# Kernel optimization log

Hardware: AMD Instinct MI355X
Metric: run time of the kernel (lower is better)

The kernel has to match this reference:

```python
import jax, jax.numpy as jnp
import numpy as np

N_NODES = 50000
N_EDGES = 800000


def _gat_conv(x, src, dst, n, W, a_src, a_dst, b, concat):
    # x: [N, Fin]; W: [Fin, H*C]; a_src/a_dst: [H, C]; b: [H*C] or [C]
    H, C = a_src.shape
    h = (x @ W).reshape(n, H, C)                     # [N,H,C]
    alpha_src = jnp.sum(h * a_src[None], axis=-1)    # [N,H]
    alpha_dst = jnp.sum(h * a_dst[None], axis=-1)    # [N,H]
    e = alpha_src[src] + alpha_dst[dst]              # [E,H]
    e = jax.nn.leaky_relu(e, negative_slope=0.2)
    # segment softmax over incoming edges of each dst node
    m = jax.ops.segment_max(e, dst, num_segments=n)  # [N,H]
    ex = jnp.exp(e - m[dst])
    s = jax.ops.segment_sum(ex, dst, num_segments=n)
    alpha = ex / (s[dst] + 1e-16)                    # [E,H]
    msg = h[src] * alpha[:, :, None]                 # [E,H,C]
    out = jax.ops.segment_sum(msg, dst, num_segments=n)  # [N,H,C]
    out = out.reshape(n, H * C) if concat else out.mean(axis=1)
    return out + b


def setup_inputs() -> dict:
    key = jax.random.key(0)
    ks = jax.random.split(key, 12)
    d = {}
    d['x'] = jax.random.normal(ks[0], (N_NODES, 128), dtype=jnp.float32)
    d['edge_index'] = jax.random.randint(ks[1], (2, N_EDGES), 0, N_NODES, dtype=jnp.int32)
    s = 0.1
    d['w1'] = jax.random.normal(ks[2], (128, 128), dtype=jnp.float32) * s
    d['att_src1'] = jax.random.normal(ks[3], (2, 64), dtype=jnp.float32) * s
    d['att_dst1'] = jax.random.normal(ks[4], (2, 64), dtype=jnp.float32) * s
    d['b1'] = jnp.zeros((128,), jnp.float32)
    d['w2'] = jax.random.normal(ks[5], (128, 128), dtype=jnp.float32) * s
    d['att_src2'] = jax.random.normal(ks[6], (2, 64), dtype=jnp.float32) * s
    d['att_dst2'] = jax.random.normal(ks[7], (2, 64), dtype=jnp.float32) * s
    d['b2'] = jnp.zeros((128,), jnp.float32)
    d['w3'] = jax.random.normal(ks[8], (128, 40), dtype=jnp.float32) * s
    d['att_src3'] = jax.random.normal(ks[9], (1, 40), dtype=jnp.float32) * s
    d['att_dst3'] = jax.random.normal(ks[10], (1, 40), dtype=jnp.float32) * s
    d['b3'] = jnp.zeros((40,), jnp.float32)
    return d


def reference(x, edge_index, w1, att_src1, att_dst1, b1,
              w2, att_src2, att_dst2, b2, w3, att_src3, att_dst3, b3):
    n = x.shape[0]
    # PyG GATConv adds self-loops by default
    loop = jnp.arange(n, dtype=edge_index.dtype)
    src = jnp.concatenate([edge_index[0], loop])
    dst = jnp.concatenate([edge_index[1], loop])
    h = _gat_conv(x, src, dst, n, w1, att_src1, att_dst1, b1, concat=True)
    h = jax.nn.elu(h)  # dropout skipped (eval mode)
    h = _gat_conv(h, src, dst, n, w2, att_src2, att_dst2, b2, concat=True)
    h = jax.nn.elu(h)
    out = _gat_conv(h, src, dst, n, w3, att_src3, att_dst3, b3, concat=False)
    return out
```

## Files before the change

### kernel.cpp

```cpp
#include <hip/hip_runtime.h>
#include <hip/hip_fp16.h>

#define NN 50000
#define NE 800000
#define E2 850000
#define SCAN_NB 49
#define GEMM_BLKS 782

static inline int cdiv(long long a, int b) { return (int)((a + b - 1) / b); }

using half8  = __attribute__((ext_vector_type(8))) _Float16;
using floatx4 = __attribute__((ext_vector_type(4))) float;

struct __align__(16) h2x4 { __half2 a, b, c, d; };
struct __align__(8)  h2x2 { __half2 a, b; };

__device__ __forceinline__ void edge_sd(const int* __restrict__ ei, int e, int& s, int& d) {
    if (e < NE) { s = ei[e]; d = ei[NE + e]; }
    else { s = e - NE; d = s; }
}

__global__ __launch_bounds__(256) void prep(const float* __restrict__ x, __half* __restrict__ x16,
                                            const float* __restrict__ w1, __half* __restrict__ wt1,
                                            const float* __restrict__ w2, __half* __restrict__ wt2,
                                            const float* __restrict__ w3, __half* __restrict__ wt3,
                                            int* __restrict__ deg) {
    int tid = blockIdx.x * 256 + threadIdx.x;
    int stride = gridDim.x * 256;
    for (int i = tid; i < NN * 32; i += stride) {
        float4 v = *(const float4*)&x[(size_t)i * 4];
        h2x2 st;
        st.a = __floats2half2_rn(v.x, v.y);
        st.b = __floats2half2_rn(v.z, v.w);
        *(h2x2*)&x16[(size_t)i * 4] = st;
    }
    for (int i = tid; i < 128 * 128; i += stride)
        wt1[i] = __float2half(w1[(i & 127) * 128 + (i >> 7)]);
    for (int i = tid; i < 128 * 128; i += stride)
        wt2[i] = __float2half(w2[(i & 127) * 128 + (i >> 7)]);
    for (int i = tid; i < 40 * 128; i += stride)
        wt3[i] = __float2half(w3[(i & 127) * 40 + (i >> 7)]);
    for (int i = tid; i < NN; i += stride) deg[i] = 0;
}

__global__ __launch_bounds__(256) void rank_pass(const int* __restrict__ ei,
                                                 int* __restrict__ deg,
                                                 int* __restrict__ rank) {
    int e = blockIdx.x * 256 + threadIdx.x;
    if (e >= E2) return;
    int d = (e < NE) ? ei[NE + e] : (e - NE);
    rank[e] = atomicAdd(&deg[d], 1);
}

__global__ __launch_bounds__(256) void scan1(const int* __restrict__ deg,
                                             int* __restrict__ loc,
                                             int* __restrict__ bsums) {
    __shared__ int wsum[4];
    int base = blockIdx.x * 1024 + threadIdx.x * 4;
    int4 v = make_int4(0, 0, 0, 0);
    if (base + 3 < NN) v = *(const int4*)&deg[base];
    else {
        if (base + 0 < NN) v.x = deg[base + 0];
        if (base + 1 < NN) v.y = deg[base + 1];
        if (base + 2 < NN) v.z = deg[base + 2];
    }
    v.y += v.x; v.z += v.y; v.w += v.z;
    int lane = threadIdx.x & 63;
    int wid = threadIdx.x >> 6;
    int t = v.w;
#pragma unroll
    for (int off = 1; off < 64; off <<= 1) {
        int u = __shfl_up(t, off, 64);
        if (lane >= off) t += u;
    }
    int excl = t - v.w;
    if (lane == 63) wsum[wid] = t;
    __syncthreads();
    int woff = 0;
    for (int w = 0; w < wid; ++w) woff += wsum[w];
    int add = excl + woff;
    int4 o = make_int4(v.x + add, v.y + add, v.z + add, v.w + add);
    if (base + 3 < NN) *(int4*)&loc[base] = o;
    else {
        if (base + 0 < NN) loc[base + 0] = o.x;
        if (base + 1 < NN) loc[base + 1] = o.y;
        if (base + 2 < NN) loc[base + 2] = o.z;
    }
    if (threadIdx.x == 255) bsums[blockIdx.x] = add + v.w;
}

__global__ __launch_bounds__(256) void scan23(const int* __restrict__ loc,
                                              const int* __restrict__ bsums,
                                              int* __restrict__ rowp) {
    __shared__ int sh_b[64];
    int tid = threadIdx.x;
    if (tid < 64) {
        int orig = (tid < SCAN_NB) ? bsums[tid] : 0;
        int v = orig;
#pragma unroll
        for (int off = 1; off < 64; off <<= 1) {
            int u = __shfl_up(v, off, 64);
            if (tid >= off) v += u;
        }
        sh_b[tid] = v - orig;
    }
    __syncthreads();
    int i = blockIdx.x * 256 + tid;
    if (i == 0) rowp[0] = 0;
    if (i < NN) rowp[i + 1] = loc[i] + sh_b[i >> 10];
}

template<int MOUT, int H>
__device__ __forceinline__ void gemm_body(int bid, const __half* __restrict__ X,
                                          const __half* __restrict__ WT,
                                          const float* __restrict__ aS,
                                          const float* __restrict__ aD,
                                          __half* __restrict__ Ho,
                                          float* __restrict__ osrc,
                                          float* __restrict__ odst,
                                          __half* wlds) {
    constexpr int NT = (MOUT + 15) / 16;
    constexpr int NR = NT * 16;
    const int tid = threadIdx.x;
    for (int i = tid * 8; i < MOUT * 128; i += 2048) {
        half8 v = *(const half8*)&WT[i];
        *(half8*)&wlds[(i >> 7) * 136 + (i & 127)] = v;
    }
    if (NR > MOUT) {
        for (int i = tid * 8; i < (NR - MOUT) * 128; i += 2048) {
            half8 z = {};
            *(half8*)&wlds[(MOUT + (i >> 7)) * 136 + (i & 127)] = z;
        }
    }
    __syncthreads();

    const int lane = tid & 63;
    const int wid = tid >> 6;
    const int r0 = bid * 64 + wid * 16;
    const int arow = r0 + (lane & 15);
    const int lrow = (arow < NN) ? arow : (NN - 1);
    const int koff = (lane >> 4) * 8;
    const size_t xbase = (size_t)lrow * 128 + koff;
    half8 a0 = *(const half8*)&X[xbase];
    half8 a1 = *(const half8*)&X[xbase + 32];
    half8 a2 = *(const half8*)&X[xbase + 64];
    half8 a3 = *(const half8*)&X[xbase + 96];

    floatx4 acc[NT];
#pragma unroll
    for (int t = 0; t < NT; ++t) acc[t] = (floatx4){0.f, 0.f, 0.f, 0.f};

#pragma unroll
    for (int t = 0; t < NT; ++t) {
        const __half* wp = &wlds[(t * 16 + (lane & 15)) * 136 + koff];
        half8 b0 = *(const half8*)&wp[0];
        half8 b1 = *(const half8*)&wp[32];
        half8 b2 = *(const half8*)&wp[64];
        half8 b3 = *(const half8*)&wp[96];
        acc[t] = __builtin_amdgcn_mfma_f32_16x16x32_f16(a0, b0, acc[t], 0, 0, 0);
        acc[t] = __builtin_amdgcn_mfma_f32_16x16x32_f16(a1, b1, acc[t], 0, 0, 0);
        acc[t] = __builtin_amdgcn_mfma_f32_16x16x32_f16(a2, b2, acc[t], 0, 0, 0);
        acc[t] = __builtin_amdgcn_mfma_f32_16x16x32_f16(a3, b3, acc[t], 0, 0, 0);
    }

    const int cc = lane & 15;
    const int rbase = r0 + (lane >> 4) * 4;
    float ps[H][4], pd[H][4];
#pragma unroll
    for (int h = 0; h < H; ++h)
#pragma unroll
        for (int r = 0; r < 4; ++r) { ps[h][r] = 0.f; pd[h][r] = 0.f; }

#pragma unroll
    for (int t = 0; t < NT; ++t) {
        const int col = t * 16 + cc;
        const bool cv = (col < MOUT);
        const float as_ = cv ? aS[col] : 0.f;
        const float ad_ = cv ? aD[col] : 0.f;
        const int h = (H == 2) ? (t >> 2) : 0;
#pragma unroll
        for (int r = 0; r < 4; ++r) {
            ps[h][r] = fmaf(acc[t][r], as_, ps[h][r]);
            pd[h][r] = fmaf(acc[t][r], ad_, pd[h][r]);
        }
    }

    if constexpr (MOUT == 128) {
        __syncthreads();
        const int rowbase = wid * 16;
#pragma unroll
        for (int t = 0; t < NT; ++t)
#pragma unroll
            for (int r = 0; r < 4; ++r)
                wlds[(rowbase + (lane >> 4) * 4 + r) * 136 + t * 16 + cc] =
                    __float2half(acc[t][r]);
        __syncthreads();
#pragma unroll
        for (int p2 = 0; p2 < 4; ++p2) {
            int f = (p2 * 64 + lane) * 8;
            int row = f >> 7, col = f & 127;
            h2x4 v = *(h2x4*)&wlds[(rowbase + row) * 136 + col];
            int grow = r0 + row;
            if (grow < NN) *(h2x4*)&Ho[(size_t)grow * 128 + col] = v;
        }
    } else {
#pragma unroll
        for (int t = 0; t < NT; ++t) {
            const int col = t * 16 + cc;
            const bool cv = (col < MOUT);
#pragma unroll
            for (int r = 0; r < 4; ++r) {
                const int m = rbase + r;
                if (cv && m < NN) Ho[(size_t)m * MOUT + col] = __float2half(acc[t][r]);
            }
        }
    }

#pragma unroll
    for (int off = 1; off <= 8; off <<= 1) {
#pragma unroll
        for (int h = 0; h < H; ++h)
#pragma unroll
            for (int r = 0; r < 4; ++r) {
                ps[h][r] += __shfl_xor(ps[h][r], off, 64);
                pd[h][r] += __shfl_xor(pd[h][r], off, 64);
            }
    }
    if (cc == 0) {
#pragma unroll
        for (int r = 0; r < 4; ++r) {
            const int m = rbase + r;
            if (m < NN) {
#pragma unroll
                for (int h = 0; h < H; ++h) {
                    osrc[m * H + h] = ps[h][r];
                    odst[m * H + h] = pd[h][r];
                }
            }
        }
    }
}

__global__ __launch_bounds__(256) void gemm16_k128(const __half* __restrict__ X,
                                                   const __half* __restrict__ WT,
                                                   const float* __restrict__ aS,
                                                   const float* __restrict__ aD,
                                                   __half* __restrict__ Ho,
                                                   float* __restrict__ osrc,
                                                   float* __restrict__ odst) {
    __shared__ __half wlds[128 * 136];
    gemm_body<128, 2>(blockIdx.x, X, WT, aS, aD, Ho, osrc, odst, wlds);
}

__global__ __launch_bounds__(256) void gemm16_k40(const __half* __restrict__ X,
                                                  const __half* __restrict__ WT,
                                                  const float* __restrict__ aS,
                                                  const float* __restrict__ aD,
                                                  __half* __restrict__ Ho,
                                                  float* __restrict__ osrc,
                                                  float* __restrict__ odst) {
    __shared__ __half wlds[48 * 136];
    gemm_body<40, 1>(blockIdx.x, X, WT, aS, aD, Ho, osrc, odst, wlds);
}

__global__ __launch_bounds__(256) void gemm1_scat(const __half* __restrict__ X,
                                                  const __half* __restrict__ WT,
                                                  const float* __restrict__ aS,
                                                  const float* __restrict__ aD,
                                                  __half* __restrict__ Ho,
                                                  float* __restrict__ osrc,
                                                  float* __restrict__ odst,
                                                  const int* __restrict__ ei,
                                                  const int* __restrict__ rowp,
                                                  const int* __restrict__ rank,
                                                  int* __restrict__ csr_src) {
    __shared__ __half wlds[128 * 136];
    if (blockIdx.x < GEMM_BLKS) {
        gemm_body<128, 2>(blockIdx.x, X, WT, aS, aD, Ho, osrc, odst, wlds);
        return;
    }
    int e = (blockIdx.x - GEMM_BLKS) * 256 + threadIdx.x;
    if (e >= E2) return;
    int s, d; edge_sd(ei, e, s, d);
    csr_src[rowp[d] + rank[e]] = s;
}

__global__ __launch_bounds__(256) void agg_h2(const int* __restrict__ rowp,
                                              const int* __restrict__ csr_src,
                                              const __half* __restrict__ Hf,
                                              const float* __restrict__ osrc,
                                              const float* __restrict__ odst,
                                              const float* __restrict__ bias,
                                              __half* __restrict__ outp) {
    int n = blockIdx.x * 4 + (threadIdx.x >> 6);
    if (n >= NN) return;
    int lane = threadIdx.x & 63;
    int i0 = rowp[n], i1 = rowp[n + 1];
    int c = lane & 15;
    int slot = lane >> 4;
    int c8 = c * 8;
    int h2 = c >> 3;
    float adh = odst[n * 2 + h2];
    bool pl = ((c & 7) == 0);

    float4 lo0{0.f,0.f,0.f,0.f}, hi0{0.f,0.f,0.f,0.f};
    float4 lo1{0.f,0.f,0.f,0.f}, hi1{0.f,0.f,0.f,0.f};
    float psum = 0.f;

    int idx = i0 + slot;
    for (; idx + 12 < i1; idx += 16) {
        int s0 = csr_src[idx];
        int s1 = csr_src[idx + 4];
        int s2 = csr_src[idx + 8];
        int s3 = csr_src[idx + 12];
        float e0 = osrc[s0 * 2 + h2] + adh;
        float e1 = osrc[s1 * 2 + h2] + adh;
        float e2 = osrc[s2 * 2 + h2] + adh;
        float e3 = osrc[s3 * 2 + h2] + adh;
        e0 = (e0 >= 0.f) ? e0 : 0.2f * e0;
        e1 = (e1 >= 0.f) ? e1 : 0.2f * e1;
        e2 = (e2 >= 0.f) ? e2 : 0.2f * e2;
        e3 = (e3 >= 0.f) ? e3 : 0.2f * e3;
        float p0 = __expf(e0), p1 = __expf(e1), p2 = __expf(e2), p3 = __expf(e3);
        h2x4 hv0 = *(const h2x4*)&Hf[(size_t)s0 * 128 + c8];
        h2x4 hv1 = *(const h2x4*)&Hf[(size_t)s1 * 128 + c8];
        h2x4 hv2 = *(const h2x4*)&Hf[(size_t)s2 * 128 + c8];
        h2x4 hv3 = *(const h2x4*)&Hf[(size_t)s3 * 128 + c8];
        if (pl) psum += (p0 + p1) + (p2 + p3);
        float2 f;
        f = __half22float2(hv0.a); lo0.x = fmaf(f.x, p0, lo0.x); lo0.y = fmaf(f.y, p0, lo0.y);
        f = __half22float2(hv0.b); lo0.z = fmaf(f.x, p0, lo0.z); lo0.w = fmaf(f.y, p0, lo0.w);
        f = __half22float2(hv0.c); hi0.x = fmaf(f.x, p0, hi0.x); hi0.y = fmaf(f.y, p0, hi0.y);
        f = __half22float2(hv0.d); hi0.z = fmaf(f.x, p0, hi0.z); hi0.w = fmaf(f.y, p0, hi0.w);
        f = __half22float2(hv1.a); lo0.x = fmaf(f.x, p1, lo0.x); lo0.y = fmaf(f.y, p1, lo0.y);
        f = __half22float2(hv1.b); lo0.z = fmaf(f.x, p1, lo0.z); lo0.w = fmaf(f.y, p1, lo0.w);
        f = __half22float2(hv1.c); hi0.x = fmaf(f.x, p1, hi0.x); hi0.y = fmaf(f.y, p1, hi0.y);
        f = __half22float2(hv1.d); hi0.z = fmaf(f.x, p1, hi0.z); hi0.w = fmaf(f.y, p1, hi0.w);
        f = __half22float2(hv2.a); lo1.x = fmaf(f.x, p2, lo1.x); lo1.y = fmaf(f.y, p2, lo1.y);
        f = __half22float2(hv2.b); lo1.z = fmaf(f.x, p2, lo1.z); lo1.w = fmaf(f.y, p2, lo1.w);
        f = __half22float2(hv2.c); hi1.x = fmaf(f.x, p2, hi1.x); hi1.y = fmaf(f.y, p2, hi1.y);
        f = __half22float2(hv2.d); hi1.z = fmaf(f.x, p2, hi1.z); hi1.w = fmaf(f.y, p2, hi1.w);
        f = __half22float2(hv3.a); lo1.x = fmaf(f.x, p3, lo1.x); lo1.y = fmaf(f.y, p3, lo1.y);
        f = __half22float2(hv3.b); lo1.z = fmaf(f.x, p3, lo1.z); lo1.w = fmaf(f.y, p3, lo1.w);
        f = __half22float2(hv3.c); hi1.x = fmaf(f.x, p3, hi1.x); hi1.y = fmaf(f.y, p3, hi1.y);
        f = __half22float2(hv3.d); hi1.z = fmaf(f.x, p3, hi1.z); hi1.w = fmaf(f.y, p3, hi1.w);
    }
    for (; idx < i1; idx += 4) {
        int s0 = csr_src[idx];
        float e0 = osrc[s0 * 2 + h2] + adh;
        e0 = (e0 >= 0.f) ? e0 : 0.2f * e0;
        float p0 = __expf(e0);
        h2x4 hv0 = *(const h2x4*)&Hf[(size_t)s0 * 128 + c8];
        if (pl) psum += p0;
        float2 f;
        f = __half22float2(hv0.a); lo0.x = fmaf(f.x, p0, lo0.x); lo0.y = fmaf(f.y, p0, lo0.y);
        f = __half22float2(hv0.b); lo0.z = fmaf(f.x, p0, lo0.z); lo0.w = fmaf(f.y, p0, lo0.w);
        f = __half22float2(hv0.c); hi0.x = fmaf(f.x, p0, hi0.x); hi0.y = fmaf(f.y, p0, hi0.y);
        f = __half22float2(hv0.d); hi0.z = fmaf(f.x, p0, hi0.z); hi0.w = fmaf(f.y, p0, hi0.w);
    }
    float4 lo{lo0.x + lo1.x, lo0.y + lo1.y, lo0.z + lo1.z, lo0.w + lo1.w};
    float4 hi{hi0.x + hi1.x, hi0.y + hi1.y, hi0.z + hi1.z, hi0.w + hi1.w};
#pragma unroll
    for (int off = 16; off <= 32; off <<= 1) {
        lo.x += __shfl_xor(lo.x, off, 64); lo.y += __shfl_xor(lo.y, off, 64);
        lo.z += __shfl_xor(lo.z, off, 64); lo.w += __shfl_xor(lo.w, off, 64);
        hi.x += __shfl_xor(hi.x, off, 64); hi.y += __shfl_xor(hi.y, off, 64);
        hi.z += __shfl_xor(hi.z, off, 64); hi.w += __shfl_xor(hi.w, off, 64);
        psum += __shfl_xor(psum, off, 64);
    }
    float sh = __shfl(psum, h2 * 8, 64);
    float inv = 1.f / (sh + 1e-16f);
    if (lane < 16) {
        float4 bl = *(const float4*)&bias[c8];
        float4 bh = *(const float4*)&bias[c8 + 4];
        float o0 = fmaf(lo.x, inv, bl.x), o1 = fmaf(lo.y, inv, bl.y);
        float o2 = fmaf(lo.z, inv, bl.z), o3 = fmaf(lo.w, inv, bl.w);
        float o4 = fmaf(hi.x, inv, bh.x), o5 = fmaf(hi.y, inv, bh.y);
        float o6 = fmaf(hi.z, inv, bh.z), o7 = fmaf(hi.w, inv, bh.w);
        o0 = (o0 > 0.f) ? o0 : (__expf(o0) - 1.f);
        o1 = (o1 > 0.f) ? o1 : (__expf(o1) - 1.f);
        o2 = (o2 > 0.f) ? o2 : (__expf(o2) - 1.f);
        o3 = (o3 > 0.f) ? o3 : (__expf(o3) - 1.f);
        o4 = (o4 > 0.f) ? o4 : (__expf(o4) - 1.f);
        o5 = (o5 > 0.f) ? o5 : (__expf(o5) - 1.f);
        o6 = (o6 > 0.f) ? o6 : (__expf(o6) - 1.f);
        o7 = (o7 > 0.f) ? o7 : (__expf(o7) - 1.f);
        h2x4 st;
        st.a = __floats2half2_rn(o0, o1);
        st.b = __floats2half2_rn(o2, o3);
        st.c = __floats2half2_rn(o4, o5);
        st.d = __floats2half2_rn(o6, o7);
        *(h2x4*)&outp[(size_t)n * 128 + c8] = st;
    }
}

__global__ __launch_bounds__(256) void agg_h1(const int* __restrict__ rowp,
                                              const int* __restrict__ csr_src,
                                              const __half* __restrict__ Hf,
                                              const float* __restrict__ osrc,
                                              const float* __restrict__ odst,
                                              const float* __restrict__ bias,
                                              float* __restrict__ outp) {
    int n = blockIdx.x * 4 + (threadIdx.x >> 6);
    if (n >= NN) return;
    int lane = threadIdx.x & 63;
    int i0 = rowp[n], i1 = rowp[n + 1];
    float ad = odst[n];
    int c = lane & 15;
    int slot = lane >> 4;
    bool cl = (c < 10);
    bool pl = (c == 0);
    float4 acc0{0.f,0.f,0.f,0.f}, acc1{0.f,0.f,0.f,0.f};
    float psum = 0.f;

    int idx = i0 + slot;
    for (; idx + 12 < i1; idx += 16) {
        int s0 = csr_src[idx];
        int s1 = csr_src[idx + 4];
        int s2 = csr_src[idx + 8];
        int s3 = csr_src[idx + 12];
        float e0 = osrc[s0] + ad, e1 = osrc[s1] + ad;
        float e2 = osrc[s2] + ad, e3 = osrc[s3] + ad;
        e0 = (e0 >= 0.f) ? e0 : 0.2f * e0;
        e1 = (e1 >= 0.f) ? e1 : 0.2f * e1;
        e2 = (e2 >= 0.f) ? e2 : 0.2f * e2;
        e3 = (e3 >= 0.f) ? e3 : 0.2f * e3;
        float p0 = __expf(e0), p1 = __expf(e1), p2 = __expf(e2), p3 = __expf(e3);
        if (pl) psum += (p0 + p1) + (p2 + p3);
        if (cl) {
            h2x2 hv0 = *(const h2x2*)&Hf[(size_t)s0 * 40 + c * 4];
            h2x2 hv1 = *(const h2x2*)&Hf[(size_t)s1 * 40 + c * 4];
            h2x2 hv2 = *(const h2x2*)&Hf[(size_t)s2 * 40 + c * 4];
            h2x2 hv3 = *(const h2x2*)&Hf[(size_t)s3 * 40 + c * 4];
            float2 f;
            f = __half22float2(hv0.a); acc0.x = fmaf(f.x, p0, acc0.x); acc0.y = fmaf(f.y, p0, acc0.y);
            f = __half22float2(hv0.b); acc0.z = fmaf(f.x, p0, acc0.z); acc0.w = fmaf(f.y, p0, acc0.w);
            f = __half22float2(hv1.a); acc1.x = fmaf(f.x, p1, acc1.x); acc1.y = fmaf(f.y, p1, acc1.y);
            f = __half22float2(hv1.b); acc1.z = fmaf(f.x, p1, acc1.z); acc1.w = fmaf(f.y, p1, acc1.w);
            f = __half22float2(hv2.a); acc0.x = fmaf(f.x, p2, acc0.x); acc0.y = fmaf(f.y, p2, acc0.y);
            f = __half22float2(hv2.b); acc0.z = fmaf(f.x, p2, acc0.z); acc0.w = fmaf(f.y, p2, acc0.w);
            f = __half22float2(hv3.a); acc1.x = fmaf(f.x, p3, acc1.x); acc1.y = fmaf(f.y, p3, acc1.y);
            f = __half22float2(hv3.b); acc1.z = fmaf(f.x, p3, acc1.z); acc1.w = fmaf(f.y, p3, acc1.w);
        }
    }
    for (; idx < i1; idx += 4) {
        int s0 = csr_src[idx];
        float e0 = osrc[s0] + ad;
        e0 = (e0 >= 0.f) ? e0 : 0.2f * e0;
        float p0 = __expf(e0);
        if (pl) psum += p0;
        if (cl) {
            h2x2 hv0 = *(const h2x2*)&Hf[(size_t)s0 * 40 + c * 4];
            float2 f;
            f = __half22float2(hv0.a); acc0.x = fmaf(f.x, p0, acc0.x); acc0.y = fmaf(f.y, p0, acc0.y);
            f = __half22float2(hv0.b); acc0.z = fmaf(f.x, p0, acc0.z); acc0.w = fmaf(f.y, p0, acc0.w);
        }
    }
    float4 acc{acc0.x + acc1.x, acc0.y + acc1.y, acc0.z + acc1.z, acc0.w + acc1.w};
#pragma unroll
    for (int off = 16; off <= 32; off <<= 1) {
        acc.x += __shfl_xor(acc.x, off, 64);
        acc.y += __shfl_xor(acc.y, off, 64);
        acc.z += __shfl_xor(acc.z, off, 64);
        acc.w += __shfl_xor(acc.w, off, 64);
        psum += __shfl_xor(psum, off, 64);
    }
    float sh = __shfl(psum, 0, 64);
    float inv = 1.f / (sh + 1e-16f);
    if (lane < 10) {
        float4 b = *(const float4*)&bias[lane * 4];
        float4 o;
        o.x = fmaf(acc.x, inv, b.x);
        o.y = fmaf(acc.y, inv, b.y);
        o.z = fmaf(acc.z, inv, b.z);
        o.w = fmaf(acc.w, inv, b.w);
        *(float4*)&outp[(size_t)n * 40 + lane * 4] = o;
    }
}

extern "C" void kernel_launch(void* const* d_in, const int* in_sizes, int n_in,
                              void* d_out, int out_size, void* d_ws, size_t ws_size,
                              hipStream_t stream) {
    const float* x   = (const float*)d_in[0];
    const int*   ei  = (const int*)d_in[1];
    const float* w1  = (const float*)d_in[2];
    const float* as1 = (const float*)d_in[3];
    const float* ad1 = (const float*)d_in[4];
    const float* b1  = (const float*)d_in[5];
    const float* w2  = (const float*)d_in[6];
    const float* as2 = (const float*)d_in[7];
    const float* ad2 = (const float*)d_in[8];
    const float* b2  = (const float*)d_in[9];
    const float* w3  = (const float*)d_in[10];
    const float* as3 = (const float*)d_in[11];
    const float* ad3 = (const float*)d_in[12];
    const float* b3  = (const float*)d_in[13];
    float* out = (float*)d_out;

    char* p = (char*)d_ws;
    __half* x16   = (__half*)p; p += (size_t)NN * 128 * 2;
    __half* h16   = (__half*)p; p += (size_t)NN * 128 * 2;
    __half* f16   = (__half*)p; p += (size_t)NN * 128 * 2;
    __half* wt1   = (__half*)p; p += (size_t)128 * 128 * 2;
    __half* wt2   = (__half*)p; p += (size_t)128 * 128 * 2;
    __half* wt3   = (__half*)p; p += (size_t)64 * 128 * 2;
    float*  osrc  = (float*)p;  p += (size_t)NN * 2 * 4;
    float*  odst  = (float*)p;  p += (size_t)NN * 2 * 4;
    int*    rowp  = (int*)p;    p += (size_t)(NN + 1) * 4;
    int*    deg   = (int*)p;    p += (size_t)NN * 4;
    int*    rank  = (int*)p;    p += (size_t)E2 * 4;
    int*    loc   = (int*)p;    p += (size_t)NN * 4;
    int*    bsums = (int*)p;    p += (size_t)64 * 4;
    int*    csrsrc= (int*)p;    p += (size_t)E2 * 4;

    const int edgeGrid = cdiv(E2, 256);
    const int nodeGrid = cdiv(NN, 4);

    prep<<<2048, 256, 0, stream>>>(x, x16, w1, wt1, w2, wt2, w3, wt3, deg);
    rank_pass<<<edgeGrid, 256, 0, stream>>>(ei, deg, rank);
    scan1<<<SCAN_NB, 256, 0, stream>>>(deg, loc, bsums);
    scan23<<<cdiv(NN, 256), 256, 0, stream>>>(loc, bsums, rowp);

    gemm1_scat<<<GEMM_BLKS + edgeGrid, 256, 0, stream>>>(x16, wt1, as1, ad1, h16,
                                                         osrc, odst, ei, rowp, rank, csrsrc);
    agg_h2<<<nodeGrid, 256, 0, stream>>>(rowp, csrsrc, h16, osrc, odst, b1, f16);

    gemm16_k128<<<GEMM_BLKS, 256, 0, stream>>>(f16, wt2, as2, ad2, h16, osrc, odst);
    agg_h2<<<nodeGrid, 256, 0, stream>>>(rowp, csrsrc, h16, osrc, odst, b2, f16);

    gemm16_k40<<<GEMM_BLKS, 256, 0, stream>>>(f16, wt3, as3, ad3, h16, osrc, odst);
    agg_h1<<<nodeGrid, 256, 0, stream>>>(rowp, csrsrc, h16, osrc, odst, b3, out);
}
```

Baseline: 198.8 us.

## Merge prep with rank pass, fuse scan into one kernel, unroll aggregation tails

```diff
diff --git a/kernel.cpp b/kernel.cpp
--- a/kernel.cpp
+++ b/kernel.cpp
@@ -6,6 +6,7 @@
 #define E2 850000
 #define SCAN_NB 49
 #define GEMM_BLKS 782
+#define RANK_BLKS 3321
 
 static inline int cdiv(long long a, int b) { return (int)((a + b - 1) / b); }
 
@@ -20,13 +21,24 @@
     else { s = e - NE; d = s; }
 }
 
-__global__ __launch_bounds__(256) void prep(const float* __restrict__ x, __half* __restrict__ x16,
-                                            const float* __restrict__ w1, __half* __restrict__ wt1,
-                                            const float* __restrict__ w2, __half* __restrict__ wt2,
-                                            const float* __restrict__ w3, __half* __restrict__ wt3,
-                                            int* __restrict__ deg) {
-    int tid = blockIdx.x * 256 + threadIdx.x;
-    int stride = gridDim.x * 256;
+__global__ __launch_bounds__(256) void prep_rank(const int* __restrict__ ei,
+                                                 int* __restrict__ deg,
+                                                 int* __restrict__ rank,
+                                                 const float* __restrict__ x, __half* __restrict__ x16,
+                                                 const float* __restrict__ w1, __half* __restrict__ wt1,
+                                                 const float* __restrict__ w2, __half* __restrict__ wt2,
+                                                 const float* __restrict__ w3, __half* __restrict__ wt3) {
+    int b = blockIdx.x;
+    if (b < RANK_BLKS) {
+        int e = b * 256 + threadIdx.x;
+        if (e < E2) {
+            int d = (e < NE) ? ei[NE + e] : (e - NE);
+            rank[e] = atomicAdd(&deg[d], 1);
+        }
+        return;
+    }
+    int tid = (b - RANK_BLKS) * 256 + threadIdx.x;
+    int stride = (gridDim.x - RANK_BLKS) * 256;
     for (int i = tid; i < NN * 32; i += stride) {
         float4 v = *(const float4*)&x[(size_t)i * 4];
         h2x2 st;
@@ -40,23 +52,16 @@
         wt2[i] = __float2half(w2[(i & 127) * 128 + (i >> 7)]);
     for (int i = tid; i < 40 * 128; i += stride)
         wt3[i] = __float2half(w3[(i & 127) * 40 + (i >> 7)]);
-    for (int i = tid; i < NN; i += stride) deg[i] = 0;
-}
-
-__global__ __launch_bounds__(256) void rank_pass(const int* __restrict__ ei,
-                                                 int* __restrict__ deg,
-                                                 int* __restrict__ rank) {
-    int e = blockIdx.x * 256 + threadIdx.x;
-    if (e >= E2) return;
-    int d = (e < NE) ? ei[NE + e] : (e - NE);
-    rank[e] = atomicAdd(&deg[d], 1);
-}
-
-__global__ __launch_bounds__(256) void scan1(const int* __restrict__ deg,
-                                             int* __restrict__ loc,
-                                             int* __restrict__ bsums) {
+}
+
+__global__ __launch_bounds__(256) void scan_all(const int* __restrict__ deg,
+                                                int* __restrict__ rowp,
+                                                int* __restrict__ bsums,
+                                                int* __restrict__ ctr) {
     __shared__ int wsum[4];
-    int base = blockIdx.x * 1024 + threadIdx.x * 4;
+    __shared__ int sh_pref[64];
+    int tid = threadIdx.x;
+    int base = blockIdx.x * 1024 + tid * 4;
     int4 v = make_int4(0, 0, 0, 0);
     if (base + 3 < NN) v = *(const int4*)&deg[base];
     else {
@@ -65,8 +70,8 @@
         if (base + 2 < NN) v.z = deg[base + 2];
     }
     v.y += v.x; v.z += v.y; v.w += v.z;
-    int lane = threadIdx.x & 63;
-    int wid = threadIdx.x >> 6;
+    int lane = tid & 63;
+    int wid = tid >> 6;
     int t = v.w;
 #pragma unroll
     for (int off = 1; off < 64; off <<= 1) {
@@ -79,35 +84,35 @@
     int woff = 0;
     for (int w = 0; w < wid; ++w) woff += wsum[w];
     int add = excl + woff;
-    int4 o = make_int4(v.x + add, v.y + add, v.z + add, v.w + add);
-    if (base + 3 < NN) *(int4*)&loc[base] = o;
-    else {
-        if (base + 0 < NN) loc[base + 0] = o.x;
-        if (base + 1 < NN) loc[base + 1] = o.y;
-        if (base + 2 < NN) loc[base + 2] = o.z;
-    }
-    if (threadIdx.x == 255) bsums[blockIdx.x] = add + v.w;
-}
-
-__global__ __launch_bounds__(256) void scan23(const int* __restrict__ loc,
-                                              const int* __restrict__ bsums,
-                                              int* __restrict__ rowp) {
-    __shared__ int sh_b[64];
-    int tid = threadIdx.x;
+    if (tid == 255) {
+        bsums[blockIdx.x] = add + v.w;
+        __threadfence();
+        atomicAdd(ctr, 1);
+    }
+    if (tid == 0) {
+        while (__hip_atomic_load(ctr, __ATOMIC_ACQUIRE, __HIP_MEMORY_SCOPE_AGENT) < SCAN_NB) {
+            __builtin_amdgcn_s_sleep(8);
+        }
+    }
+    __syncthreads();
     if (tid < 64) {
-        int orig = (tid < SCAN_NB) ? bsums[tid] : 0;
-        int v = orig;
+        int bv = (tid < SCAN_NB)
+            ? __hip_atomic_load(&bsums[tid], __ATOMIC_RELAXED, __HIP_MEMORY_SCOPE_AGENT) : 0;
+        int s = bv;
 #pragma unroll
         for (int off = 1; off < 64; off <<= 1) {
-            int u = __shfl_up(v, off, 64);
-            if (tid >= off) v += u;
-        }
-        sh_b[tid] = v - orig;
+            int u = __shfl_up(s, off, 64);
+            if (tid >= off) s += u;
+        }
+        sh_pref[tid] = s - bv;
     }
     __syncthreads();
-    int i = blockIdx.x * 256 + tid;
-    if (i == 0) rowp[0] = 0;
-    if (i < NN) rowp[i + 1] = loc[i] + sh_b[i >> 10];
+    int boff = sh_pref[blockIdx.x];
+    if (base == 0) rowp[0] = 0;
+    if (base + 0 < NN) rowp[base + 1] = v.x + add + boff;
+    if (base + 1 < NN) rowp[base + 2] = v.y + add + boff;
+    if (base + 2 < NN) rowp[base + 3] = v.z + add + boff;
+    if (base + 3 < NN) rowp[base + 4] = v.w + add + boff;
 }
 
 template<int MOUT, int H>
@@ -345,18 +350,39 @@
         f = __half22float2(hv3.c); hi1.x = fmaf(f.x, p3, hi1.x); hi1.y = fmaf(f.y, p3, hi1.y);
         f = __half22float2(hv3.d); hi1.z = fmaf(f.x, p3, hi1.z); hi1.w = fmaf(f.y, p3, hi1.w);
     }
-    for (; idx < i1; idx += 4) {
-        int s0 = csr_src[idx];
+    {
+        int id1 = idx + 4, id2 = idx + 8;
+        bool v0 = idx < i1, v1 = id1 < i1, v2 = id2 < i1;
+        int lim = i1 - 1;
+        int s0 = csr_src[min(idx, lim)];
+        int s1 = csr_src[min(id1, lim)];
+        int s2 = csr_src[min(id2, lim)];
         float e0 = osrc[s0 * 2 + h2] + adh;
+        float e1 = osrc[s1 * 2 + h2] + adh;
+        float e2 = osrc[s2 * 2 + h2] + adh;
         e0 = (e0 >= 0.f) ? e0 : 0.2f * e0;
-        float p0 = __expf(e0);
+        e1 = (e1 >= 0.f) ? e1 : 0.2f * e1;
+        e2 = (e2 >= 0.f) ? e2 : 0.2f * e2;
+        float p0 = v0 ? __expf(e0) : 0.f;
+        float p1 = v1 ? __expf(e1) : 0.f;
+        float p2 = v2 ? __expf(e2) : 0.f;
         h2x4 hv0 = *(const h2x4*)&Hf[(size_t)s0 * 128 + c8];
-        if (pl) psum += p0;
+        h2x4 hv1 = *(const h2x4*)&Hf[(size_t)s1 * 128 + c8];
+        h2x4 hv2 = *(const h2x4*)&Hf[(size_t)s2 * 128 + c8];
+        if (pl) psum += (p0 + p1) + p2;
         float2 f;
         f = __half22float2(hv0.a); lo0.x = fmaf(f.x, p0, lo0.x); lo0.y = fmaf(f.y, p0, lo0.y);
         f = __half22float2(hv0.b); lo0.z = fmaf(f.x, p0, lo0.z); lo0.w = fmaf(f.y, p0, lo0.w);
         f = __half22float2(hv0.c); hi0.x = fmaf(f.x, p0, hi0.x); hi0.y = fmaf(f.y, p0, hi0.y);
         f = __half22float2(hv0.d); hi0.z = fmaf(f.x, p0, hi0.z); hi0.w = fmaf(f.y, p0, hi0.w);
+        f = __half22float2(hv1.a); lo0.x = fmaf(f.x, p1, lo0.x); lo0.y = fmaf(f.y, p1, lo0.y);
+        f = __half22float2(hv1.b); lo0.z = fmaf(f.x, p1, lo0.z); lo0.w = fmaf(f.y, p1, lo0.w);
+        f = __half22float2(hv1.c); hi0.x = fmaf(f.x, p1, hi0.x); hi0.y = fmaf(f.y, p1, hi0.y);
+        f = __half22float2(hv1.d); hi0.z = fmaf(f.x, p1, hi0.z); hi0.w = fmaf(f.y, p1, hi0.w);
+        f = __half22float2(hv2.a); lo1.x = fmaf(f.x, p2, lo1.x); lo1.y = fmaf(f.y, p2, lo1.y);
+        f = __half22float2(hv2.b); lo1.z = fmaf(f.x, p2, lo1.z); lo1.w = fmaf(f.y, p2, lo1.w);
+        f = __half22float2(hv2.c); hi1.x = fmaf(f.x, p2, hi1.x); hi1.y = fmaf(f.y, p2, hi1.y);
+        f = __half22float2(hv2.d); hi1.z = fmaf(f.x, p2, hi1.z); hi1.w = fmaf(f.y, p2, hi1.w);
     }
     float4 lo{lo0.x + lo1.x, lo0.y + lo1.y, lo0.z + lo1.z, lo0.w + lo1.w};
     float4 hi{hi0.x + hi1.x, hi0.y + hi1.y, hi0.z + hi1.z, hi0.w + hi1.w};
@@ -443,17 +469,32 @@
             f = __half22float2(hv3.b); acc1.z = fmaf(f.x, p3, acc1.z); acc1.w = fmaf(f.y, p3, acc1.w);
         }
     }
-    for (; idx < i1; idx += 4) {
-        int s0 = csr_src[idx];
-        float e0 = osrc[s0] + ad;
+    {
+        int id1 = idx + 4, id2 = idx + 8;
+        bool v0 = idx < i1, v1 = id1 < i1, v2 = id2 < i1;
+        int lim = i1 - 1;
+        int s0 = csr_src[min(idx, lim)];
+        int s1 = csr_src[min(id1, lim)];
+        int s2 = csr_src[min(id2, lim)];
+        float e0 = osrc[s0] + ad, e1 = osrc[s1] + ad, e2 = osrc[s2] + ad;
         e0 = (e0 >= 0.f) ? e0 : 0.2f * e0;
-        float p0 = __expf(e0);
-        if (pl) psum += p0;
+        e1 = (e1 >= 0.f) ? e1 : 0.2f * e1;
+        e2 = (e2 >= 0.f) ? e2 : 0.2f * e2;
+        float p0 = v0 ? __expf(e0) : 0.f;
+        float p1 = v1 ? __expf(e1) : 0.f;
+        float p2 = v2 ? __expf(e2) : 0.f;
+        if (pl) psum += (p0 + p1) + p2;
         if (cl) {
             h2x2 hv0 = *(const h2x2*)&Hf[(size_t)s0 * 40 + c * 4];
+            h2x2 hv1 = *(const h2x2*)&Hf[(size_t)s1 * 40 + c * 4];
+            h2x2 hv2 = *(const h2x2*)&Hf[(size_t)s2 * 40 + c * 4];
             float2 f;
             f = __half22float2(hv0.a); acc0.x = fmaf(f.x, p0, acc0.x); acc0.y = fmaf(f.y, p0, acc0.y);
             f = __half22float2(hv0.b); acc0.z = fmaf(f.x, p0, acc0.z); acc0.w = fmaf(f.y, p0, acc0.w);
+            f = __half22float2(hv1.a); acc1.x = fmaf(f.x, p1, acc1.x); acc1.y = fmaf(f.y, p1, acc1.y);
+            f = __half22float2(hv1.b); acc1.z = fmaf(f.x, p1, acc1.z); acc1.w = fmaf(f.y, p1, acc1.w);
+            f = __half22float2(hv2.a); acc0.x = fmaf(f.x, p2, acc0.x); acc0.y = fmaf(f.y, p2, acc0.y);
+            f = __half22float2(hv2.b); acc0.z = fmaf(f.x, p2, acc0.z); acc0.w = fmaf(f.y, p2, acc0.w);
         }
     }
     float4 acc{acc0.x + acc1.x, acc0.y + acc1.y, acc0.z + acc1.z, acc0.w + acc1.w};
@@ -508,18 +549,18 @@
     float*  odst  = (float*)p;  p += (size_t)NN * 2 * 4;
     int*    rowp  = (int*)p;    p += (size_t)(NN + 1) * 4;
     int*    deg   = (int*)p;    p += (size_t)NN * 4;
+    int*    ctr   = (int*)p;    p += (size_t)4;
     int*    rank  = (int*)p;    p += (size_t)E2 * 4;
-    int*    loc   = (int*)p;    p += (size_t)NN * 4;
     int*    bsums = (int*)p;    p += (size_t)64 * 4;
     int*    csrsrc= (int*)p;    p += (size_t)E2 * 4;
 
     const int edgeGrid = cdiv(E2, 256);
     const int nodeGrid = cdiv(NN, 4);
 
-    prep<<<2048, 256, 0, stream>>>(x, x16, w1, wt1, w2, wt2, w3, wt3, deg);
-    rank_pass<<<edgeGrid, 256, 0, stream>>>(ei, deg, rank);
-    scan1<<<SCAN_NB, 256, 0, stream>>>(deg, loc, bsums);
-    scan23<<<cdiv(NN, 256), 256, 0, stream>>>(loc, bsums, rowp);
+    hipMemsetAsync(deg, 0, (size_t)(NN + 1) * 4, stream);
+    prep_rank<<<RANK_BLKS + 1024, 256, 0, stream>>>(ei, deg, rank, x, x16,
+                                                    w1, wt1, w2, wt2, w3, wt3);
+    scan_all<<<SCAN_NB, 256, 0, stream>>>(deg, rowp, bsums, ctr);
 
     gemm1_scat<<<GEMM_BLKS + edgeGrid, 256, 0, stream>>>(x16, wt1, as1, ad1, h16,
                                                          osrc, odst, ei, rowp, rank, csrsrc);
```

Measured after the change: 200.1 us. About the same (+0.6%).
